# Performance work log

Measured on AMD Instinct MI355X. Metric: run time of the kernel, lower is better.

Reference implementation:

```python
import jax, jax.numpy as jnp
import numpy as np

H, C = 2, 128           # heads, out_channels per head
HC = H * C              # 256 concat output dim
D_IN = 256              # in_channels
D_T = 128               # time encoder out_channels
D_MSG = 128
E_DIM = D_MSG + D_T     # edge_dim = 256
N = 50000
E = 200000
MEAN_DT, STD_DT = 0.0, 1.0
SQRT_C = np.float32(np.sqrt(C))


def _time_enc(rel_t, W_t, b_t):
    # TGN TimeEncoder: cos(Linear(rel_t.view(-1,1)))  -> [E, D_T]
    return jnp.cos(rel_t[:, None] * W_t[0] + b_t)


def _seg_softmax(alpha, dst, n_dst):
    # numerically stable scatter-softmax over destination-node segments
    amax = jax.ops.segment_max(alpha, dst, num_segments=n_dst)
    amax = jnp.where(jnp.isfinite(amax), amax, 0.0)
    ex = jnp.exp(alpha - amax[dst])
    denom = jax.ops.segment_sum(ex, dst, num_segments=n_dst)
    return ex / (denom[dst] + 1e-16)


def _transformer_conv(x_src, x_dst, ei, edge_attr, Wq, bq, Wk, bk, Wv, bv, We, Ws, bs):
    n_dst = x_dst.shape[0]
    src, dst = ei[0], ei[1]
    q = (x_dst @ Wq + bq).reshape(n_dst, H, C)
    k = ((x_src @ Wk + bk)[src]).reshape(-1, H, C)      # gather per edge
    v = ((x_src @ Wv + bv)[src]).reshape(-1, H, C)
    e = (edge_attr @ We).reshape(-1, H, C)              # lin_edge (no bias)
    alpha = jnp.sum(q[dst] * (k + e), axis=-1) / SQRT_C  # [E, H]
    alpha = _seg_softmax(alpha, dst, n_dst)
    msg = (v + e) * alpha[..., None]                    # [E, H, C]
    out = jax.ops.segment_sum(msg.reshape(-1, HC), dst, num_segments=n_dst)
    return out + x_dst @ Ws + bs                        # root/skip connection


def setup_inputs() -> dict:
    key = jax.random.key(0)
    ks = jax.random.split(key, 32)
    s = 0.05
    inp = {
        'x_user': jax.random.normal(ks[0], (N, D_IN), jnp.float32),
        'x_item': jax.random.normal(ks[1], (N, D_IN), jnp.float32),
        'last_update_user': jax.random.uniform(ks[2], (N,), jnp.float32) * 100.0,
        'last_update_item': jax.random.uniform(ks[3], (N,), jnp.float32) * 100.0,
        'edge_index_a': jax.random.randint(ks[4], (2, E), 0, N, jnp.int32),
        'edge_index_b': jax.random.randint(ks[5], (2, E), 0, N, jnp.int32),
        't_a': jax.random.uniform(ks[6], (E,), jnp.float32) * 100.0 + 100.0,
        't_b': jax.random.uniform(ks[7], (E,), jnp.float32) * 100.0 + 100.0,
        'msg_a': jax.random.normal(ks[8], (E, D_MSG), jnp.float32),
        'msg_b': jax.random.normal(ks[9], (E, D_MSG), jnp.float32),
        'W_t': jax.random.normal(ks[10], (1, D_T), jnp.float32) * s,
        'b_t': jax.random.normal(ks[11], (D_T,), jnp.float32) * s,
    }
    i = 12
    for suf in ('a', 'b'):
        for nm, shape in (('Wq', (D_IN, HC)), ('bq', (HC,)), ('Wk', (D_IN, HC)), ('bk', (HC,)),
                          ('Wv', (D_IN, HC)), ('bv', (HC,)), ('We', (E_DIM, HC)),
                          ('Ws', (D_IN, HC)), ('bs', (HC,))):
            inp[f'{nm}_{suf}'] = jax.random.normal(ks[i], shape, jnp.float32) * s
            i += 1
    return inp


def reference(x_user, x_item, last_update_user, last_update_item,
              edge_index_a, edge_index_b, t_a, t_b, msg_a, msg_b, W_t, b_t,
              Wq_a, bq_a, Wk_a, bk_a, Wv_a, bv_a, We_a, Ws_a, bs_a,
              Wq_b, bq_b, Wk_b, bk_b, Wv_b, bv_b, We_b, Ws_b, bs_b):
    # edge type a: ('user','to','item');  edge type b: ('item','rev_to','user')
    rel_a = (t_a - last_update_user[edge_index_a[0]] - MEAN_DT) / STD_DT
    ea = jnp.concatenate([_time_enc(rel_a, W_t, b_t), msg_a], axis=-1)
    rel_b = (t_b - last_update_item[edge_index_b[0]] - MEAN_DT) / STD_DT
    eb = jnp.concatenate([_time_enc(rel_b, W_t, b_t), msg_b], axis=-1)
    out_item = _transformer_conv(x_user, x_item, edge_index_a, ea,
                                 Wq_a, bq_a, Wk_a, bk_a, Wv_a, bv_a, We_a, Ws_a, bs_a)
    out_user = _transformer_conv(x_item, x_user, edge_index_b, eb,
                                 Wq_b, bq_b, Wk_b, bk_b, Wv_b, bv_b, We_b, Ws_b, bs_b)
    return out_user, out_item
```

## Files before the change

kernel.cpp:

```cpp
#include <hip/hip_runtime.h>
#include <hip/hip_bf16.h>

#define N_NODES 50000
#define E_EDGES 200000
static constexpr float INV_SQRT_C = 0.08838834764831845f;
static constexpr int NB_NODE = ((N_NODES + 63) / 64) * 4;
static constexpr int NB_EDGE = E_EDGES / 64;
static constexpr int NB_PAIR = 2 * NB_EDGE;
static constexpr int NB_FUSED = NB_NODE + NB_EDGE;

typedef __attribute__((ext_vector_type(4))) float f32x4;
typedef __attribute__((ext_vector_type(8))) short s16x8;
typedef __attribute__((ext_vector_type(4))) short s16x4;

__device__ __forceinline__ float b2f(unsigned short u) {
  union { unsigned u; float f; } x; x.u = ((unsigned)u) << 16; return x.f;
}
__device__ __forceinline__ short f2b(float f) {
  union { float f; unsigned u; } x; x.f = f;
  unsigned r = x.u + 0x7FFFu + ((x.u >> 16) & 1u);
  return (short)(r >> 16);
}

struct WPtrs { const float* w[10]; };

__global__ __launch_bounds__(256) void prep_transpose(WPtrs p, short* __restrict__ out) {
  __shared__ short T[256 * 66];
  const int wi = blockIdx.x >> 2, cq = blockIdx.x & 3;
  const float* w = p.w[wi];
  short* o = out + wi * 65536;
  const int tid = threadIdx.x;
#pragma unroll
  for (int i = 0; i < 64; ++i) {
    int flat = tid + i * 256;
    int k = flat >> 6, cc = flat & 63;
    T[k * 66 + cc] = f2b(w[k * 256 + cq * 64 + cc]);
  }
  __syncthreads();
#pragma unroll
  for (int i = 0; i < 8; ++i) {
    int flat2 = tid + i * 256;
    int g = flat2 & 3, colb = (flat2 >> 2) & 15, ks = (flat2 >> 6) & 7, ctl = flat2 >> 9;
    int ct = cq * 4 + ctl;
    s16x8 v;
#pragma unroll
    for (int j = 0; j < 8; ++j)
      v[j] = T[(ks * 32 + g * 8 + j) * 66 + ctl * 16 + colb];
    *(s16x8*)(o + (((ct * 8 + ks) * 16 + colb) * 32 + g * 8)) = v;
  }
}

__global__ __launch_bounds__(256) void conv_x(const float* __restrict__ xu,
                                              const float* __restrict__ xi,
                                              unsigned short* __restrict__ x16u,
                                              unsigned short* __restrict__ x16i) {
  const float* in = blockIdx.y ? xi : xu;
  unsigned short* out = blockIdx.y ? x16i : x16u;
  size_t base = ((size_t)blockIdx.x * 256 + threadIdx.x) * 8;
  float4 a = *(const float4*)(in + base);
  float4 b = *(const float4*)(in + base + 4);
  s16x8 v;
  v[0] = f2b(a.x); v[1] = f2b(a.y); v[2] = f2b(a.z); v[3] = f2b(a.w);
  v[4] = f2b(b.x); v[5] = f2b(b.y); v[6] = f2b(b.z); v[7] = f2b(b.w);
  *(s16x8*)(out + base) = v;
}

__global__ __launch_bounds__(256) void csr_count2(const int* __restrict__ eia,
                                                  const int* __restrict__ eib,
                                                  int* __restrict__ counts) {
  int t = blockIdx.x * 256 + threadIdx.x;
  const int* ei = blockIdx.y ? eib : eia;
  int* c = counts + blockIdx.y * N_NODES;
  if (t < E_EDGES) atomicAdd(&c[ei[E_EDGES + t]], 1);
}

__global__ __launch_bounds__(1024) void csr_scan2(int* __restrict__ counts,
                                                  int* __restrict__ start) {
  int* cnt = counts + blockIdx.x * N_NODES;
  int* st  = start + blockIdx.x * (N_NODES + 1);
  __shared__ int wsum[16];
  __shared__ int chunk_tot;
  __shared__ int carry_s;
  const int tid = threadIdx.x, lane = tid & 63, wid = tid >> 6;
  if (tid == 0) carry_s = 0;
  __syncthreads();
  for (int base = 0; base < N_NODES; base += 1024) {
    int gi = base + tid;
    int x = (gi < N_NODES) ? cnt[gi] : 0;
    int v = x;
#pragma unroll
    for (int d = 1; d < 64; d <<= 1) {
      int t = __shfl_up(v, d);
      if (lane >= d) v += t;
    }
    if (lane == 63) wsum[wid] = v;
    __syncthreads();
    if (tid == 0) {
      int run = 0;
#pragma unroll
      for (int i = 0; i < 16; ++i) { int t = wsum[i]; wsum[i] = run; run += t; }
      chunk_tot = run;
    }
    __syncthreads();
    if (gi < N_NODES) {
      int excl = carry_s + wsum[wid] + v - x;
      st[gi] = excl;
      cnt[gi] = excl;
    }
    __syncthreads();
    if (tid == 0) carry_s += chunk_tot;
  }
  if (tid == 0) st[N_NODES] = carry_s;
}

__global__ __launch_bounds__(256) void csr_fill2(const int* __restrict__ eia,
                                                 const int* __restrict__ eib,
                                                 int* __restrict__ counts,
                                                 int* __restrict__ pos,
                                                 unsigned short* __restrict__ esrc) {
  int t = blockIdx.x * 256 + threadIdx.x;
  const int* ei = blockIdx.y ? eib : eia;
  int* cur = counts + blockIdx.y * N_NODES;
  int* ps  = pos + blockIdx.y * E_EDGES;
  unsigned short* es = esrc + (size_t)blockIdx.y * E_EDGES;
  if (t < E_EDGES) {
    int d = ei[E_EDGES + t];
    int p = atomicAdd(&cur[d], 1);
    ps[t] = p;
    es[p] = (unsigned short)ei[t];
  }
}

struct FusedArgs {
  const unsigned short* X16[4];
  const float* Xf[4];
  const short* Wt[4];
  const float* bias[4];
  unsigned short* o16[4];
  float* of[4];
  int use16;
  const int* ei; const float* tvec; const float* lu; const float* msg;
  const float* Wtim; const float* btim; const short* WeT; const int* pos;
  unsigned short* e16g;
};

__global__ __launch_bounds__(512) void fused_ne(FusedArgs A) {
  __shared__ __align__(16) char smem[34816];
  const int bx = blockIdx.x;
  const int tid = threadIdx.x;
  const int l = tid & 63;
  const int w = tid >> 6;
  const int colb = l & 15;
  const int g = l >> 4;

  int nb = -1, eb = -1;
  if (bx < NB_PAIR) { if (bx & 1) eb = bx >> 1; else nb = bx >> 1; }
  else nb = NB_EDGE + (bx - NB_PAIR);

  if (nb >= 0) {
    short* As = (short*)smem;
    const int job = nb / 782;
    const int m0 = (nb - job * 782) * 64;
    const bool fullblk = (m0 + 64 <= N_NODES);
    const short* Wt = A.Wt[job];
    const float* bias = A.bias[job];
    unsigned short* o16 = A.o16[job];
    float* of = A.of[job];

    if (A.use16) {
      const unsigned short* X = A.X16[job];
      if (fullblk) {
#pragma unroll
        for (int i = 0; i < 4; ++i) {
          int flat = tid + i * 512;
          int r = flat >> 5, cg = flat & 31;
          *(s16x8*)&As[r * 264 + cg * 8] = *(const s16x8*)(X + (size_t)(m0 + r) * 256 + cg * 8);
        }
      } else {
#pragma unroll
        for (int i = 0; i < 4; ++i) {
          int flat = tid + i * 512;
          int r = flat >> 5, cg = flat & 31;
          s16x8 v = (s16x8)(short)0;
          if (m0 + r < N_NODES) v = *(const s16x8*)(X + (size_t)(m0 + r) * 256 + cg * 8);
          *(s16x8*)&As[r * 264 + cg * 8] = v;
        }
      }
    } else {
      const float* X = A.Xf[job];
#pragma unroll
      for (int i = 0; i < 8; ++i) {
        int flat = tid + i * 512;
        int r = flat >> 6, c4 = flat & 63;
        float4 xv = make_float4(0.f, 0.f, 0.f, 0.f);
        if (fullblk || m0 + r < N_NODES) xv = *(const float4*)(X + (size_t)(m0 + r) * 256 + c4 * 4);
        s16x4 sv; sv[0] = f2b(xv.x); sv[1] = f2b(xv.y); sv[2] = f2b(xv.z); sv[3] = f2b(xv.w);
        *(s16x4*)&As[r * 264 + c4 * 4] = sv;
      }
    }
    __syncthreads();

    const short* wbase0 = Wt + (((2 * w + 0) * 8) * 16 + colb) * 32 + g * 8;
    const short* wbase1 = Wt + (((2 * w + 1) * 8) * 16 + colb) * 32 + g * 8;

    f32x4 acc[4][2];
#pragma unroll
    for (int m = 0; m < 4; ++m) { acc[m][0] = (f32x4)(0.0f); acc[m][1] = (f32x4)(0.0f); }
#pragma unroll
    for (int ks = 0; ks < 8; ++ks) {
      s16x8 b0 = *(const s16x8*)(wbase0 + ks * 512);
      s16x8 b1 = *(const s16x8*)(wbase1 + ks * 512);
#pragma unroll
      for (int m = 0; m < 4; ++m) {
        s16x8 a = *(const s16x8*)&As[(16 * m + colb) * 264 + ks * 32 + g * 8];
        acc[m][0] = __builtin_amdgcn_mfma_f32_16x16x32_bf16(a, b0, acc[m][0], 0, 0, 0);
        acc[m][1] = __builtin_amdgcn_mfma_f32_16x16x32_bf16(a, b1, acc[m][1], 0, 0, 0);
      }
    }
    __syncthreads();

    if (of) {
      float* buf = (float*)smem;
#pragma unroll 1
      for (int half = 0; half < 2; ++half) {
#pragma unroll
        for (int j = 0; j < 2; ++j) {
          int col = (2 * w + j) * 16 + colb;
          float bv = bias[col];
#pragma unroll
          for (int mm = 0; mm < 2; ++mm) {
            int m = half * 2 + mm;
#pragma unroll
            for (int r = 0; r < 4; ++r)
              buf[(16 * mm + g * 4 + r) * 260 + col] = acc[m][j][r] + bv;
          }
        }
        __syncthreads();
#pragma unroll
        for (int i = 0; i < 4; ++i) {
          int flat = tid + i * 512;
          int row = flat >> 6, ch = flat & 63;
          int grow = m0 + half * 32 + row;
          if (fullblk || grow < N_NODES)
            *(float4*)(of + (size_t)grow * 256 + ch * 4) = *(const float4*)&buf[row * 260 + ch * 4];
        }
        __syncthreads();
      }
    } else {
      short* buf = (short*)smem;
#pragma unroll
      for (int j = 0; j < 2; ++j) {
        int col = (2 * w + j) * 16 + colb;
        float bv = bias[col];
#pragma unroll
        for (int m = 0; m < 4; ++m)
#pragma unroll
          for (int r = 0; r < 4; ++r)
            buf[(16 * m + g * 4 + r) * 264 + col] = f2b(acc[m][j][r] + bv);
      }
      __syncthreads();
#pragma unroll
      for (int i = 0; i < 4; ++i) {
        int flat = tid + i * 512;
        int row = flat >> 5, ch = flat & 31;
        if (fullblk || m0 + row < N_NODES)
          *(s16x8*)(o16 + (size_t)(m0 + row) * 256 + ch * 8) = *(const s16x8*)&buf[row * 264 + ch * 8];
      }
    }
  } else {
    short* attr = (short*)smem;
    float* rel  = (float*)(smem + 33792);
    int*   poss = (int*)(smem + 34048);
    const int e0 = eb * 64;

    const float wt = A.Wtim[tid & 127], bt = A.btim[tid & 127];

    if (tid < 64) {
      rel[tid] = A.tvec[e0 + tid] - A.lu[A.ei[e0 + tid]];
      poss[tid] = A.pos[e0 + tid];
    }
#pragma unroll
    for (int i = 0; i < 4; ++i) {
      int flat = tid + i * 512;
      int row = flat >> 5, c4 = flat & 31;
      float4 mv = *(const float4*)(A.msg + (size_t)(e0 + row) * 128 + c4 * 4);
      s16x4 sv; sv[0] = f2b(mv.x); sv[1] = f2b(mv.y); sv[2] = f2b(mv.z); sv[3] = f2b(mv.w);
      *(s16x4*)&attr[row * 264 + 128 + c4 * 4] = sv;
    }
    __syncthreads();

    {
      int col = tid & 127;
      int r0 = (tid >> 7) * 16;
#pragma unroll
      for (int i = 0; i < 16; ++i)
        attr[(r0 + i) * 264 + col] = f2b(__cosf(rel[r0 + i] * wt + bt));
    }
    __syncthreads();

    const short* wbase0 = A.WeT + (((2 * w + 0) * 8) * 16 + colb) * 32 + g * 8;
    const short* wbase1 = A.WeT + (((2 * w + 1) * 8) * 16 + colb) * 32 + g * 8;
    f32x4 acc[4][2];
#pragma unroll
    for (int m = 0; m < 4; ++m) { acc[m][0] = (f32x4)(0.0f); acc[m][1] = (f32x4)(0.0f); }
#pragma unroll
    for (int ks = 0; ks < 8; ++ks) {
      s16x8 b0 = *(const s16x8*)(wbase0 + ks * 512);
      s16x8 b1 = *(const s16x8*)(wbase1 + ks * 512);
#pragma unroll
      for (int m = 0; m < 4; ++m) {
        s16x8 a = *(const s16x8*)&attr[(16 * m + colb) * 264 + ks * 32 + g * 8];
        acc[m][0] = __builtin_amdgcn_mfma_f32_16x16x32_bf16(a, b0, acc[m][0], 0, 0, 0);
        acc[m][1] = __builtin_amdgcn_mfma_f32_16x16x32_bf16(a, b1, acc[m][1], 0, 0, 0);
      }
    }
    __syncthreads();
#pragma unroll
    for (int j = 0; j < 2; ++j)
#pragma unroll
      for (int m = 0; m < 4; ++m)
#pragma unroll
        for (int r = 0; r < 4; ++r)
          attr[(16 * m + g * 4 + r) * 264 + (2 * w + j) * 16 + colb] = f2b(acc[m][j][r]);
    __syncthreads();

#pragma unroll
    for (int i = 0; i < 4; ++i) {
      int flat = tid + i * 512;
      int row = flat >> 5, cg = flat & 31;
      size_t slot = (size_t)poss[row];
      *(s16x8*)(A.e16g + slot * 256 + cg * 8) = *(const s16x8*)&attr[row * 264 + cg * 8];
    }
  }
}

__global__ __launch_bounds__(256) void aggregate_fused5(
    const int* __restrict__ start, const unsigned short* __restrict__ esrc,
    const unsigned short* __restrict__ Q16, const unsigned short* __restrict__ K16,
    const unsigned short* __restrict__ V16, const unsigned short* __restrict__ e16,
    float* __restrict__ out)
{
  const int wave = blockIdx.x * 4 + (threadIdx.x >> 6);
  const int nwaves = gridDim.x * 4;
  const int lane = threadIdx.x & 63;
  const int c0 = lane * 4;

  for (int d = wave; d < N_NODES; d += nwaves) {
    const int s0 = start[d], s1 = start[d + 1];
    if (s1 <= s0) continue;

    s16x4 qv = *(const s16x4*)(Q16 + (size_t)d * 256 + c0);
    const float q0 = b2f((unsigned short)qv[0]), q1 = b2f((unsigned short)qv[1]);
    const float q2 = b2f((unsigned short)qv[2]), q3 = b2f((unsigned short)qv[3]);

    float den = 0.f;
    float a0 = 0.f, a1 = 0.f, a2 = 0.f, a3 = 0.f;
    int p = s0;

#define EDGE_LOAD(J, PP)                                                    \
    int s##J = (int)esrc[PP];                                               \
    s16x4 ev##J = *(const s16x4*)(e16 + (size_t)(PP) * 256 + c0);           \
    s16x4 kv##J = *(const s16x4*)(K16 + (size_t)s##J * 256 + c0);           \
    s16x4 vv##J = *(const s16x4*)(V16 + (size_t)s##J * 256 + c0);           \
    float e0##J = b2f((unsigned short)ev##J[0]), e1##J = b2f((unsigned short)ev##J[1]); \
    float e2##J = b2f((unsigned short)ev##J[2]), e3##J = b2f((unsigned short)ev##J[3]); \
    float dt##J = q0 * (b2f((unsigned short)kv##J[0]) + e0##J)              \
                + q1 * (b2f((unsigned short)kv##J[1]) + e1##J)              \
                + q2 * (b2f((unsigned short)kv##J[2]) + e2##J)              \
                + q3 * (b2f((unsigned short)kv##J[3]) + e3##J);

#define EDGE_ACC(J)                                                         \
    den += ex##J;                                                           \
    a0 += ex##J * (b2f((unsigned short)vv##J[0]) + e0##J);                  \
    a1 += ex##J * (b2f((unsigned short)vv##J[1]) + e1##J);                  \
    a2 += ex##J * (b2f((unsigned short)vv##J[2]) + e2##J);                  \
    a3 += ex##J * (b2f((unsigned short)vv##J[3]) + e3##J);

    for (; p + 4 <= s1; p += 4) {
      EDGE_LOAD(A, p)  EDGE_LOAD(B, p + 1)  EDGE_LOAD(C, p + 2)  EDGE_LOAD(D, p + 3)
      dtA += __shfl_xor(dtA, 1);  dtB += __shfl_xor(dtB, 1);
      dtC += __shfl_xor(dtC, 1);  dtD += __shfl_xor(dtD, 1);
      dtA += __shfl_xor(dtA, 2);  dtB += __shfl_xor(dtB, 2);
      dtC += __shfl_xor(dtC, 2);  dtD += __shfl_xor(dtD, 2);
      dtA += __shfl_xor(dtA, 4);  dtB += __shfl_xor(dtB, 4);
      dtC += __shfl_xor(dtC, 4);  dtD += __shfl_xor(dtD, 4);
      dtA += __shfl_xor(dtA, 8);  dtB += __shfl_xor(dtB, 8);
      dtC += __shfl_xor(dtC, 8);  dtD += __shfl_xor(dtD, 8);
      dtA += __shfl_xor(dtA, 16); dtB += __shfl_xor(dtB, 16);
      dtC += __shfl_xor(dtC, 16); dtD += __shfl_xor(dtD, 16);
      float exA = __expf(dtA * INV_SQRT_C), exB = __expf(dtB * INV_SQRT_C);
      float exC = __expf(dtC * INV_SQRT_C), exD = __expf(dtD * INV_SQRT_C);
      EDGE_ACC(A) EDGE_ACC(B) EDGE_ACC(C) EDGE_ACC(D)
    }
    for (; p < s1; ++p) {
      EDGE_LOAD(T, p)
      dtT += __shfl_xor(dtT, 1);
      dtT += __shfl_xor(dtT, 2);
      dtT += __shfl_xor(dtT, 4);
      dtT += __shfl_xor(dtT, 8);
      dtT += __shfl_xor(dtT, 16);
      float exT = __expf(dtT * INV_SQRT_C);
      EDGE_ACC(T)
    }
#undef EDGE_LOAD
#undef EDGE_ACC

    float inv = 1.f / (den + 1e-16f);
    float4* op = (float4*)(out + (size_t)d * 256 + c0);
    float4 o = *op;
    o.x += a0 * inv; o.y += a1 * inv; o.z += a2 * inv; o.w += a3 * inv;
    *op = o;
  }
}

extern "C" void kernel_launch(void* const* d_in, const int* in_sizes, int n_in,
                              void* d_out, int out_size, void* d_ws, size_t ws_size,
                              hipStream_t stream) {
  const float* x_user  = (const float*)d_in[0];
  const float* x_item  = (const float*)d_in[1];
  const float* lu_user = (const float*)d_in[2];
  const float* lu_item = (const float*)d_in[3];
  const int*   ei_a    = (const int*)d_in[4];
  const int*   ei_b    = (const int*)d_in[5];
  const float* t_a     = (const float*)d_in[6];
  const float* t_b     = (const float*)d_in[7];
  const float* msg_a   = (const float*)d_in[8];
  const float* msg_b   = (const float*)d_in[9];
  const float* W_t     = (const float*)d_in[10];
  const float* b_t     = (const float*)d_in[11];
  const float* Wq_a = (const float*)d_in[12]; const float* bq_a = (const float*)d_in[13];
  const float* Wk_a = (const float*)d_in[14]; const float* bk_a = (const float*)d_in[15];
  const float* Wv_a = (const float*)d_in[16]; const float* bv_a = (const float*)d_in[17];
  const float* We_a = (const float*)d_in[18];
  const float* Ws_a = (const float*)d_in[19]; const float* bs_a = (const float*)d_in[20];
  const float* Wq_b = (const float*)d_in[21]; const float* bq_b = (const float*)d_in[22];
  const float* Wk_b = (const float*)d_in[23]; const float* bk_b = (const float*)d_in[24];
  const float* Wv_b = (const float*)d_in[25]; const float* bv_b = (const float*)d_in[26];
  const float* We_b = (const float*)d_in[27];
  const float* Ws_b = (const float*)d_in[28]; const float* bs_b = (const float*)d_in[29];

  float* out_user = (float*)d_out;
  float* out_item = (float*)d_out + (size_t)N_NODES * 256;

  WPtrs wp;
  wp.w[0] = Wq_a; wp.w[1] = Wk_a; wp.w[2] = Wv_a; wp.w[3] = Ws_a; wp.w[4] = We_a;
  wp.w[5] = Wq_b; wp.w[6] = Wk_b; wp.w[7] = Wv_b; wp.w[8] = Ws_b; wp.w[9] = We_b;

  dim3 blk(256);
  dim3 blk512(512);
  dim3 gW(40);
  dim3 gF(NB_FUSED);
  dim3 gEt2((E_EDGES + 255) / 256, 2);
  dim3 gAgg(1024);
  dim3 gCv(6250, 2);

  char* ws = (char*)d_ws;
  size_t off = 0;
  short* WtT = (short*)(ws + off); off += (size_t)10 * 65536 * 2;
  unsigned short* Q16 = (unsigned short*)(ws + off); off += (size_t)N_NODES * 256 * 2;
  unsigned short* K16 = (unsigned short*)(ws + off); off += (size_t)N_NODES * 256 * 2;
  unsigned short* V16 = (unsigned short*)(ws + off); off += (size_t)N_NODES * 256 * 2;
  unsigned short* e16 = (unsigned short*)(ws + off); off += (size_t)E_EDGES * 256 * 2;
  int* pos    = (int*)(ws + off); off += (size_t)2 * E_EDGES * 4;
  int* counts = (int*)(ws + off); off += (size_t)2 * N_NODES * 4;
  int* startb = (int*)(ws + off); off += (size_t)2 * (N_NODES + 1) * 4;
  unsigned short* esrc = (unsigned short*)(ws + off); off += (size_t)2 * E_EDGES * 2;
  const size_t off_base = off;
  unsigned short* X16u = (unsigned short*)(ws + off); off += (size_t)N_NODES * 256 * 2;
  unsigned short* X16i = (unsigned short*)(ws + off); off += (size_t)N_NODES * 256 * 2;
  const bool use_x16 = (ws_size >= off);
  if (!use_x16 && ws_size < off_base) return;

  prep_transpose<<<gW, blk, 0, stream>>>(wp, WtT);

  hipMemsetAsync(counts, 0, (size_t)2 * N_NODES * 4, stream);
  csr_count2<<<gEt2, blk, 0, stream>>>(ei_a, ei_b, counts);
  csr_scan2<<<2, 1024, 0, stream>>>(counts, startb);
  csr_fill2<<<gEt2, blk, 0, stream>>>(ei_a, ei_b, counts, pos, esrc);

  if (use_x16)
    conv_x<<<gCv, blk, 0, stream>>>(x_user, x_item, X16u, X16i);

  {
    FusedArgs Aa;
    Aa.X16[0] = X16u; Aa.X16[1] = X16u; Aa.X16[2] = X16i; Aa.X16[3] = X16i;
    Aa.Xf[0] = x_user; Aa.Xf[1] = x_user; Aa.Xf[2] = x_item; Aa.Xf[3] = x_item;
    Aa.Wt[0] = WtT + 1 * 65536; Aa.Wt[1] = WtT + 2 * 65536;
    Aa.Wt[2] = WtT + 0 * 65536; Aa.Wt[3] = WtT + 3 * 65536;
    Aa.bias[0] = bk_a; Aa.bias[1] = bv_a; Aa.bias[2] = bq_a; Aa.bias[3] = bs_a;
    Aa.o16[0] = K16; Aa.o16[1] = V16; Aa.o16[2] = Q16; Aa.o16[3] = nullptr;
    Aa.of[0] = nullptr; Aa.of[1] = nullptr; Aa.of[2] = nullptr; Aa.of[3] = out_item;
    Aa.use16 = use_x16 ? 1 : 0;
    Aa.ei = ei_a; Aa.tvec = t_a; Aa.lu = lu_user; Aa.msg = msg_a;
    Aa.Wtim = W_t; Aa.btim = b_t; Aa.WeT = WtT + 4 * 65536; Aa.pos = pos;
    Aa.e16g = e16;
    fused_ne<<<gF, blk512, 0, stream>>>(Aa);
  }
  aggregate_fused5<<<gAgg, blk, 0, stream>>>(startb, esrc, Q16, K16, V16, e16, out_item);

  {
    FusedArgs Ab;
    Ab.X16[0] = X16i; Ab.X16[1] = X16i; Ab.X16[2] = X16u; Ab.X16[3] = X16u;
    Ab.Xf[0] = x_item; Ab.Xf[1] = x_item; Ab.Xf[2] = x_user; Ab.Xf[3] = x_user;
    Ab.Wt[0] = WtT + 6 * 65536; Ab.Wt[1] = WtT + 7 * 65536;
    Ab.Wt[2] = WtT + 5 * 65536; Ab.Wt[3] = WtT + 8 * 65536;
    Ab.bias[0] = bk_b; Ab.bias[1] = bv_b; Ab.bias[2] = bq_b; Ab.bias[3] = bs_b;
    Ab.o16[0] = K16; Ab.o16[1] = V16; Ab.o16[2] = Q16; Ab.o16[3] = nullptr;
    Ab.of[0] = nullptr; Ab.of[1] = nullptr; Ab.of[2] = nullptr; Ab.of[3] = out_user;
    Ab.use16 = use_x16 ? 1 : 0;
    Ab.ei = ei_b; Ab.tvec = t_b; Ab.lu = lu_item; Ab.msg = msg_b;
    Ab.Wtim = W_t; Ab.btim = b_t; Ab.WeT = WtT + 9 * 65536; Ab.pos = pos + E_EDGES;
    Ab.e16g = e16;
    fused_ne<<<gF, blk512, 0, stream>>>(Ab);
  }
  aggregate_fused5<<<gAgg, blk, 0, stream>>>(startb + (N_NODES + 1), esrc + E_EDGES,
      Q16, K16, V16, e16, out_user);
}
```

Baseline: 587.0 us.

## Merge both edge types into single projection and aggregation kernels

Adds a second set of Q/K/V/edge-feature workspace buffers so both edge types can be processed together. Their projection GEMMs then run in one mega_ne launch and their aggregations in one mega_agg launch, interleaving destinations of both types. Weight transpose, bf16 conversion of x and CSR counting are folded into a single setup kernel. The aim is to remove launch gaps and serialization between the two convolutions and fill the GPU better, at the cost of more workspace memory, with a fallback to the old path when workspace is too small.

```diff
diff --git a/kernel.cpp b/kernel.cpp
--- a/kernel.cpp
+++ b/kernel.cpp
@@ -8,6 +8,9 @@
 static constexpr int NB_EDGE = E_EDGES / 64;
 static constexpr int NB_PAIR = 2 * NB_EDGE;
 static constexpr int NB_FUSED = NB_NODE + NB_EDGE;
+static constexpr int NB_PREP = 40;
+static constexpr int NB_CONV = 12500;
+static constexpr int NB_CNT  = ((E_EDGES + 255) / 256) * 2;
 
 typedef __attribute__((ext_vector_type(4))) float f32x4;
 typedef __attribute__((ext_vector_type(8))) short s16x8;
@@ -24,53 +27,335 @@
 
 struct WPtrs { const float* w[10]; };
 
-__global__ __launch_bounds__(256) void prep_transpose(WPtrs p, short* __restrict__ out) {
+struct NodeSet {
+  const unsigned short* X16[4];
+  const float* Xf[4];
+  const short* Wt[4];
+  const float* bias[4];
+  unsigned short* o16[4];
+  float* of[4];
+};
+struct EdgeSet {
+  const int* ei; const float* tvec; const float* lu; const float* msg;
+  const short* WeT; const int* pos; unsigned short* e16g;
+};
+
+__device__ __forceinline__ void node_block(char* smem, int tid, int nb,
+                                           const NodeSet& N, int use16) {
+  short* As = (short*)smem;
+  const int l = tid & 63;
+  const int w = tid >> 6;
+  const int colb = l & 15;
+  const int g = l >> 4;
+  const int job = nb / 782;
+  const int m0 = (nb - job * 782) * 64;
+  const bool fullblk = (m0 + 64 <= N_NODES);
+  const short* Wt = N.Wt[job];
+  const float* bias = N.bias[job];
+  unsigned short* o16 = N.o16[job];
+  float* of = N.of[job];
+
+  if (use16) {
+    const unsigned short* X = N.X16[job];
+    if (fullblk) {
+#pragma unroll
+      for (int i = 0; i < 4; ++i) {
+        int flat = tid + i * 512;
+        int r = flat >> 5, cg = flat & 31;
+        *(s16x8*)&As[r * 264 + cg * 8] = *(const s16x8*)(X + (size_t)(m0 + r) * 256 + cg * 8);
+      }
+    } else {
+#pragma unroll
+      for (int i = 0; i < 4; ++i) {
+        int flat = tid + i * 512;
+        int r = flat >> 5, cg = flat & 31;
+        s16x8 v = (s16x8)(short)0;
+        if (m0 + r < N_NODES) v = *(const s16x8*)(X + (size_t)(m0 + r) * 256 + cg * 8);
+        *(s16x8*)&As[r * 264 + cg * 8] = v;
+      }
+    }
+  } else {
+    const float* X = N.Xf[job];
+#pragma unroll
+    for (int i = 0; i < 8; ++i) {
+      int flat = tid + i * 512;
+      int r = flat >> 6, c4 = flat & 63;
+      float4 xv = make_float4(0.f, 0.f, 0.f, 0.f);
+      if (fullblk || m0 + r < N_NODES) xv = *(const float4*)(X + (size_t)(m0 + r) * 256 + c4 * 4);
+      s16x4 sv; sv[0] = f2b(xv.x); sv[1] = f2b(xv.y); sv[2] = f2b(xv.z); sv[3] = f2b(xv.w);
+      *(s16x4*)&As[r * 264 + c4 * 4] = sv;
+    }
+  }
+  __syncthreads();
+
+  const short* wbase0 = Wt + (((2 * w + 0) * 8) * 16 + colb) * 32 + g * 8;
+  const short* wbase1 = Wt + (((2 * w + 1) * 8) * 16 + colb) * 32 + g * 8;
+
+  f32x4 acc[4][2];
+#pragma unroll
+  for (int m = 0; m < 4; ++m) { acc[m][0] = (f32x4)(0.0f); acc[m][1] = (f32x4)(0.0f); }
+#pragma unroll
+  for (int ks = 0; ks < 8; ++ks) {
+    s16x8 b0 = *(const s16x8*)(wbase0 + ks * 512);
+    s16x8 b1 = *(const s16x8*)(wbase1 + ks * 512);
+#pragma unroll
+    for (int m = 0; m < 4; ++m) {
+      s16x8 a = *(const s16x8*)&As[(16 * m + colb) * 264 + ks * 32 + g * 8];
+      acc[m][0] = __builtin_amdgcn_mfma_f32_16x16x32_bf16(a, b0, acc[m][0], 0, 0, 0);
+      acc[m][1] = __builtin_amdgcn_mfma_f32_16x16x32_bf16(a, b1, acc[m][1], 0, 0, 0);
+    }
+  }
+  __syncthreads();
+
+  if (of) {
+    float* buf = (float*)smem;
+#pragma unroll 1
+    for (int half = 0; half < 2; ++half) {
+#pragma unroll
+      for (int j = 0; j < 2; ++j) {
+        int col = (2 * w + j) * 16 + colb;
+        float bv = bias[col];
+#pragma unroll
+        for (int mm = 0; mm < 2; ++mm) {
+          int m = half * 2 + mm;
+#pragma unroll
+          for (int r = 0; r < 4; ++r)
+            buf[(16 * mm + g * 4 + r) * 260 + col] = acc[m][j][r] + bv;
+        }
+      }
+      __syncthreads();
+#pragma unroll
+      for (int i = 0; i < 4; ++i) {
+        int flat = tid + i * 512;
+        int row = flat >> 6, ch = flat & 63;
+        int grow = m0 + half * 32 + row;
+        if (fullblk || grow < N_NODES)
+          *(float4*)(of + (size_t)grow * 256 + ch * 4) = *(const float4*)&buf[row * 260 + ch * 4];
+      }
+      __syncthreads();
+    }
+  } else {
+    short* buf = (short*)smem;
+#pragma unroll
+    for (int j = 0; j < 2; ++j) {
+      int col = (2 * w + j) * 16 + colb;
+      float bv = bias[col];
+#pragma unroll
+      for (int m = 0; m < 4; ++m)
+#pragma unroll
+        for (int r = 0; r < 4; ++r)
+          buf[(16 * m + g * 4 + r) * 264 + col] = f2b(acc[m][j][r] + bv);
+    }
+    __syncthreads();
+#pragma unroll
+    for (int i = 0; i < 4; ++i) {
+      int flat = tid + i * 512;
+      int row = flat >> 5, ch = flat & 31;
+      if (fullblk || m0 + row < N_NODES)
+        *(s16x8*)(o16 + (size_t)(m0 + row) * 256 + ch * 8) = *(const s16x8*)&buf[row * 264 + ch * 8];
+    }
+  }
+}
+
+__device__ __forceinline__ void edge_block(char* smem, int tid, int eb,
+                                           const EdgeSet& E,
+                                           const float* Wtim, const float* btim) {
+  short* attr = (short*)smem;
+  float* rel  = (float*)(smem + 33792);
+  int*   poss = (int*)(smem + 34048);
+  const int l = tid & 63;
+  const int w = tid >> 6;
+  const int colb = l & 15;
+  const int g = l >> 4;
+  const int e0 = eb * 64;
+
+  const float wt = Wtim[tid & 127], bt = btim[tid & 127];
+
+  if (tid < 64) {
+    rel[tid] = E.tvec[e0 + tid] - E.lu[E.ei[e0 + tid]];
+    poss[tid] = E.pos[e0 + tid];
+  }
+#pragma unroll
+  for (int i = 0; i < 4; ++i) {
+    int flat = tid + i * 512;
+    int row = flat >> 5, c4 = flat & 31;
+    float4 mv = *(const float4*)(E.msg + (size_t)(e0 + row) * 128 + c4 * 4);
+    s16x4 sv; sv[0] = f2b(mv.x); sv[1] = f2b(mv.y); sv[2] = f2b(mv.z); sv[3] = f2b(mv.w);
+    *(s16x4*)&attr[row * 264 + 128 + c4 * 4] = sv;
+  }
+  __syncthreads();
+
+  {
+    int col = tid & 127;
+    int r0 = (tid >> 7) * 16;
+#pragma unroll
+    for (int i = 0; i < 16; ++i)
+      attr[(r0 + i) * 264 + col] = f2b(__cosf(rel[r0 + i] * wt + bt));
+  }
+  __syncthreads();
+
+  const short* wbase0 = E.WeT + (((2 * w + 0) * 8) * 16 + colb) * 32 + g * 8;
+  const short* wbase1 = E.WeT + (((2 * w + 1) * 8) * 16 + colb) * 32 + g * 8;
+  f32x4 acc[4][2];
+#pragma unroll
+  for (int m = 0; m < 4; ++m) { acc[m][0] = (f32x4)(0.0f); acc[m][1] = (f32x4)(0.0f); }
+#pragma unroll
+  for (int ks = 0; ks < 8; ++ks) {
+    s16x8 b0 = *(const s16x8*)(wbase0 + ks * 512);
+    s16x8 b1 = *(const s16x8*)(wbase1 + ks * 512);
+#pragma unroll
+    for (int m = 0; m < 4; ++m) {
+      s16x8 a = *(const s16x8*)&attr[(16 * m + colb) * 264 + ks * 32 + g * 8];
+      acc[m][0] = __builtin_amdgcn_mfma_f32_16x16x32_bf16(a, b0, acc[m][0], 0, 0, 0);
+      acc[m][1] = __builtin_amdgcn_mfma_f32_16x16x32_bf16(a, b1, acc[m][1], 0, 0, 0);
+    }
+  }
+  __syncthreads();
+#pragma unroll
+  for (int j = 0; j < 2; ++j)
+#pragma unroll
+    for (int m = 0; m < 4; ++m)
+#pragma unroll
+      for (int r = 0; r < 4; ++r)
+        attr[(16 * m + g * 4 + r) * 264 + (2 * w + j) * 16 + colb] = f2b(acc[m][j][r]);
+  __syncthreads();
+
+#pragma unroll
+  for (int i = 0; i < 4; ++i) {
+    int flat = tid + i * 512;
+    int row = flat >> 5, cg = flat & 31;
+    size_t slot = (size_t)poss[row];
+    *(s16x8*)(E.e16g + slot * 256 + cg * 8) = *(const s16x8*)&attr[row * 264 + cg * 8];
+  }
+}
+
+__device__ __forceinline__ void process_dst(
+    int d, int c0, const int* __restrict__ start, const unsigned short* __restrict__ esrc,
+    const unsigned short* __restrict__ Q16, const unsigned short* __restrict__ K16,
+    const unsigned short* __restrict__ V16, const unsigned short* __restrict__ e16,
+    float* __restrict__ out)
+{
+  const int s0 = start[d], s1 = start[d + 1];
+  if (s1 <= s0) return;
+
+  s16x4 qv = *(const s16x4*)(Q16 + (size_t)d * 256 + c0);
+  const float q0 = b2f((unsigned short)qv[0]), q1 = b2f((unsigned short)qv[1]);
+  const float q2 = b2f((unsigned short)qv[2]), q3 = b2f((unsigned short)qv[3]);
+
+  float den = 0.f;
+  float a0 = 0.f, a1 = 0.f, a2 = 0.f, a3 = 0.f;
+  int p = s0;
+
+#define EDGE_LOAD(J, PP)                                                    \
+    int s##J = (int)esrc[PP];                                               \
+    s16x4 ev##J = *(const s16x4*)(e16 + (size_t)(PP) * 256 + c0);           \
+    s16x4 kv##J = *(const s16x4*)(K16 + (size_t)s##J * 256 + c0);           \
+    s16x4 vv##J = *(const s16x4*)(V16 + (size_t)s##J * 256 + c0);           \
+    float e0##J = b2f((unsigned short)ev##J[0]), e1##J = b2f((unsigned short)ev##J[1]); \
+    float e2##J = b2f((unsigned short)ev##J[2]), e3##J = b2f((unsigned short)ev##J[3]); \
+    float dt##J = q0 * (b2f((unsigned short)kv##J[0]) + e0##J)              \
+                + q1 * (b2f((unsigned short)kv##J[1]) + e1##J)              \
+                + q2 * (b2f((unsigned short)kv##J[2]) + e2##J)              \
+                + q3 * (b2f((unsigned short)kv##J[3]) + e3##J);
+
+#define EDGE_ACC(J)                                                         \
+    den += ex##J;                                                           \
+    a0 += ex##J * (b2f((unsigned short)vv##J[0]) + e0##J);                  \
+    a1 += ex##J * (b2f((unsigned short)vv##J[1]) + e1##J);                  \
+    a2 += ex##J * (b2f((unsigned short)vv##J[2]) + e2##J);                  \
+    a3 += ex##J * (b2f((unsigned short)vv##J[3]) + e3##J);
+
+  for (; p + 4 <= s1; p += 4) {
+    EDGE_LOAD(A, p)  EDGE_LOAD(B, p + 1)  EDGE_LOAD(C, p + 2)  EDGE_LOAD(D, p + 3)
+    dtA += __shfl_xor(dtA, 1);  dtB += __shfl_xor(dtB, 1);
+    dtC += __shfl_xor(dtC, 1);  dtD += __shfl_xor(dtD, 1);
+    dtA += __shfl_xor(dtA, 2);  dtB += __shfl_xor(dtB, 2);
+    dtC += __shfl_xor(dtC, 2);  dtD += __shfl_xor(dtD, 2);
+    dtA += __shfl_xor(dtA, 4);  dtB += __shfl_xor(dtB, 4);
+    dtC += __shfl_xor(dtC, 4);  dtD += __shfl_xor(dtD, 4);
+    dtA += __shfl_xor(dtA, 8);  dtB += __shfl_xor(dtB, 8);
+    dtC += __shfl_xor(dtC, 8);  dtD += __shfl_xor(dtD, 8);
+    dtA += __shfl_xor(dtA, 16); dtB += __shfl_xor(dtB, 16);
+    dtC += __shfl_xor(dtC, 16); dtD += __shfl_xor(dtD, 16);
+    float exA = __expf(dtA * INV_SQRT_C), exB = __expf(dtB * INV_SQRT_C);
+    float exC = __expf(dtC * INV_SQRT_C), exD = __expf(dtD * INV_SQRT_C);
+    EDGE_ACC(A) EDGE_ACC(B) EDGE_ACC(C) EDGE_ACC(D)
+  }
+  for (; p < s1; ++p) {
+    EDGE_LOAD(T, p)
+    dtT += __shfl_xor(dtT, 1);
+    dtT += __shfl_xor(dtT, 2);
+    dtT += __shfl_xor(dtT, 4);
+    dtT += __shfl_xor(dtT, 8);
+    dtT += __shfl_xor(dtT, 16);
+    float exT = __expf(dtT * INV_SQRT_C);
+    EDGE_ACC(T)
+  }
+#undef EDGE_LOAD
+#undef EDGE_ACC
+
+  float inv = 1.f / (den + 1e-16f);
+  float4* op = (float4*)(out + (size_t)d * 256 + c0);
+  float4 o = *op;
+  o.x += a0 * inv; o.y += a1 * inv; o.z += a2 * inv; o.w += a3 * inv;
+  *op = o;
+}
+
+__global__ __launch_bounds__(256) void setup_fused(
+    WPtrs p, short* __restrict__ WtT,
+    const float* __restrict__ xu, const float* __restrict__ xi,
+    unsigned short* __restrict__ x16u, unsigned short* __restrict__ x16i, int nconv,
+    const int* __restrict__ eia, const int* __restrict__ eib, int* __restrict__ counts)
+{
   __shared__ short T[256 * 66];
-  const int wi = blockIdx.x >> 2, cq = blockIdx.x & 3;
-  const float* w = p.w[wi];
-  short* o = out + wi * 65536;
+  const int bx = blockIdx.x;
   const int tid = threadIdx.x;
-#pragma unroll
-  for (int i = 0; i < 64; ++i) {
-    int flat = tid + i * 256;
-    int k = flat >> 6, cc = flat & 63;
-    T[k * 66 + cc] = f2b(w[k * 256 + cq * 64 + cc]);
-  }
-  __syncthreads();
-#pragma unroll
-  for (int i = 0; i < 8; ++i) {
-    int flat2 = tid + i * 256;
-    int g = flat2 & 3, colb = (flat2 >> 2) & 15, ks = (flat2 >> 6) & 7, ctl = flat2 >> 9;
-    int ct = cq * 4 + ctl;
+
+  if (bx < NB_PREP) {
+    const int wi = bx >> 2, cq = bx & 3;
+    const float* w = p.w[wi];
+    short* o = WtT + wi * 65536;
+#pragma unroll
+    for (int i = 0; i < 64; ++i) {
+      int flat = tid + i * 256;
+      int k = flat >> 6, cc = flat & 63;
+      T[k * 66 + cc] = f2b(w[k * 256 + cq * 64 + cc]);
+    }
+    __syncthreads();
+#pragma unroll
+    for (int i = 0; i < 8; ++i) {
+      int flat2 = tid + i * 256;
+      int g = flat2 & 3, colb = (flat2 >> 2) & 15, ks = (flat2 >> 6) & 7, ctl = flat2 >> 9;
+      int ct = cq * 4 + ctl;
+      s16x8 v;
+#pragma unroll
+      for (int j = 0; j < 8; ++j)
+        v[j] = T[(ks * 32 + g * 8 + j) * 66 + ctl * 16 + colb];
+      *(s16x8*)(o + (((ct * 8 + ks) * 16 + colb) * 32 + g * 8)) = v;
+    }
+    return;
+  }
+  int cb = bx - NB_PREP;
+  if (cb < nconv) {
+    int y = cb >= (nconv / 2);
+    int xb = y ? cb - nconv / 2 : cb;
+    const float* in = y ? xi : xu;
+    unsigned short* out = y ? x16i : x16u;
+    size_t base = ((size_t)xb * 256 + tid) * 8;
+    float4 a = *(const float4*)(in + base);
+    float4 b = *(const float4*)(in + base + 4);
     s16x8 v;
-#pragma unroll
-    for (int j = 0; j < 8; ++j)
-      v[j] = T[(ks * 32 + g * 8 + j) * 66 + ctl * 16 + colb];
-    *(s16x8*)(o + (((ct * 8 + ks) * 16 + colb) * 32 + g * 8)) = v;
-  }
-}
-
-__global__ __launch_bounds__(256) void conv_x(const float* __restrict__ xu,
-                                              const float* __restrict__ xi,
-                                              unsigned short* __restrict__ x16u,
-                                              unsigned short* __restrict__ x16i) {
-  const float* in = blockIdx.y ? xi : xu;
-  unsigned short* out = blockIdx.y ? x16i : x16u;
-  size_t base = ((size_t)blockIdx.x * 256 + threadIdx.x) * 8;
-  float4 a = *(const float4*)(in + base);
-  float4 b = *(const float4*)(in + base + 4);
-  s16x8 v;
-  v[0] = f2b(a.x); v[1] = f2b(a.y); v[2] = f2b(a.z); v[3] = f2b(a.w);
-  v[4] = f2b(b.x); v[5] = f2b(b.y); v[6] = f2b(b.z); v[7] = f2b(b.w);
-  *(s16x8*)(out + base) = v;
-}
-
-__global__ __launch_bounds__(256) void csr_count2(const int* __restrict__ eia,
-                                                  const int* __restrict__ eib,
-                                                  int* __restrict__ counts) {
-  int t = blockIdx.x * 256 + threadIdx.x;
-  const int* ei = blockIdx.y ? eib : eia;
-  int* c = counts + blockIdx.y * N_NODES;
+    v[0] = f2b(a.x); v[1] = f2b(a.y); v[2] = f2b(a.z); v[3] = f2b(a.w);
+    v[4] = f2b(b.x); v[5] = f2b(b.y); v[6] = f2b(b.z); v[7] = f2b(b.w);
+    *(s16x8*)(out + base) = v;
+    return;
+  }
+  cb -= nconv;
+  int y = cb >= (NB_CNT / 2);
+  int tb = y ? cb - NB_CNT / 2 : cb;
+  const int* ei = y ? eib : eia;
+  int* c = counts + y * N_NODES;
+  int t = tb * 256 + tid;
   if (t < E_EDGES) atomicAdd(&c[ei[E_EDGES + t]], 1);
 }
 
@@ -131,207 +416,29 @@
   }
 }
 
-struct FusedArgs {
-  const unsigned short* X16[4];
-  const float* Xf[4];
-  const short* Wt[4];
-  const float* bias[4];
-  unsigned short* o16[4];
-  float* of[4];
-  int use16;
-  const int* ei; const float* tvec; const float* lu; const float* msg;
-  const float* Wtim; const float* btim; const short* WeT; const int* pos;
-  unsigned short* e16g;
-};
+struct FusedArgs { NodeSet n; EdgeSet e; const float* Wtim; const float* btim; int use16; };
 
 __global__ __launch_bounds__(512) void fused_ne(FusedArgs A) {
   __shared__ __align__(16) char smem[34816];
   const int bx = blockIdx.x;
-  const int tid = threadIdx.x;
-  const int l = tid & 63;
-  const int w = tid >> 6;
-  const int colb = l & 15;
-  const int g = l >> 4;
-
   int nb = -1, eb = -1;
   if (bx < NB_PAIR) { if (bx & 1) eb = bx >> 1; else nb = bx >> 1; }
   else nb = NB_EDGE + (bx - NB_PAIR);
-
-  if (nb >= 0) {
-    short* As = (short*)smem;
-    const int job = nb / 782;
-    const int m0 = (nb - job * 782) * 64;
-    const bool fullblk = (m0 + 64 <= N_NODES);
-    const short* Wt = A.Wt[job];
-    const float* bias = A.bias[job];
-    unsigned short* o16 = A.o16[job];
-    float* of = A.of[job];
-
-    if (A.use16) {
-      const unsigned short* X = A.X16[job];
-      if (fullblk) {
-#pragma unroll
-        for (int i = 0; i < 4; ++i) {
-          int flat = tid + i * 512;
-          int r = flat >> 5, cg = flat & 31;
-          *(s16x8*)&As[r * 264 + cg * 8] = *(const s16x8*)(X + (size_t)(m0 + r) * 256 + cg * 8);
-        }
-      } else {
-#pragma unroll
-        for (int i = 0; i < 4; ++i) {
-          int flat = tid + i * 512;
-          int r = flat >> 5, cg = flat & 31;
-          s16x8 v = (s16x8)(short)0;
-          if (m0 + r < N_NODES) v = *(const s16x8*)(X + (size_t)(m0 + r) * 256 + cg * 8);
-          *(s16x8*)&As[r * 264 + cg * 8] = v;
-        }
-      }
-    } else {
-      const float* X = A.Xf[job];
-#pragma unroll
-      for (int i = 0; i < 8; ++i) {
-        int flat = tid + i * 512;
-        int r = flat >> 6, c4 = flat & 63;
-        float4 xv = make_float4(0.f, 0.f, 0.f, 0.f);
-        if (fullblk || m0 + r < N_NODES) xv = *(const float4*)(X + (size_t)(m0 + r) * 256 + c4 * 4);
-        s16x4 sv; sv[0] = f2b(xv.x); sv[1] = f2b(xv.y); sv[2] = f2b(xv.z); sv[3] = f2b(xv.w);
-        *(s16x4*)&As[r * 264 + c4 * 4] = sv;
-      }
-    }
-    __syncthreads();
-
-    const short* wbase0 = Wt + (((2 * w + 0) * 8) * 16 + colb) * 32 + g * 8;
-    const short* wbase1 = Wt + (((2 * w + 1) * 8) * 16 + colb) * 32 + g * 8;
-
-    f32x4 acc[4][2];
-#pragma unroll
-    for (int m = 0; m < 4; ++m) { acc[m][0] = (f32x4)(0.0f); acc[m][1] = (f32x4)(0.0f); }
-#pragma unroll
-    for (int ks = 0; ks < 8; ++ks) {
-      s16x8 b0 = *(const s16x8*)(wbase0 + ks * 512);
-      s16x8 b1 = *(const s16x8*)(wbase1 + ks * 512);
-#pragma unroll
-      for (int m = 0; m < 4; ++m) {
-        s16x8 a = *(const s16x8*)&As[(16 * m + colb) * 264 + ks * 32 + g * 8];
-        acc[m][0] = __builtin_amdgcn_mfma_f32_16x16x32_bf16(a, b0, acc[m][0], 0, 0, 0);
-        acc[m][1] = __builtin_amdgcn_mfma_f32_16x16x32_bf16(a, b1, acc[m][1], 0, 0, 0);
-      }
-    }
-    __syncthreads();
-
-    if (of) {
-      float* buf = (float*)smem;
-#pragma unroll 1
-      for (int half = 0; half < 2; ++half) {
-#pragma unroll
-        for (int j = 0; j < 2; ++j) {
-          int col = (2 * w + j) * 16 + colb;
-          float bv = bias[col];
-#pragma unroll
-          for (int mm = 0; mm < 2; ++mm) {
-            int m = half * 2 + mm;
-#pragma unroll
-            for (int r = 0; r < 4; ++r)
-              buf[(16 * mm + g * 4 + r) * 260 + col] = acc[m][j][r] + bv;
-          }
-        }
-        __syncthreads();
-#pragma unroll
-        for (int i = 0; i < 4; ++i) {
-          int flat = tid + i * 512;
-          int row = flat >> 6, ch = flat & 63;
-          int grow = m0 + half * 32 + row;
-          if (fullblk || grow < N_NODES)
-            *(float4*)(of + (size_t)grow * 256 + ch * 4) = *(const float4*)&buf[row * 260 + ch * 4];
-        }
-        __syncthreads();
-      }
-    } else {
-      short* buf = (short*)smem;
-#pragma unroll
-      for (int j = 0; j < 2; ++j) {
-        int col = (2 * w + j) * 16 + colb;
-        float bv = bias[col];
-#pragma unroll
-        for (int m = 0; m < 4; ++m)
-#pragma unroll
-          for (int r = 0; r < 4; ++r)
-            buf[(16 * m + g * 4 + r) * 264 + col] = f2b(acc[m][j][r] + bv);
-      }
-      __syncthreads();
-#pragma unroll
-      for (int i = 0; i < 4; ++i) {
-        int flat = tid + i * 512;
-        int row = flat >> 5, ch = flat & 31;
-        if (fullblk || m0 + row < N_NODES)
-          *(s16x8*)(o16 + (size_t)(m0 + row) * 256 + ch * 8) = *(const s16x8*)&buf[row * 264 + ch * 8];
-      }
-    }
-  } else {
-    short* attr = (short*)smem;
-    float* rel  = (float*)(smem + 33792);
-    int*   poss = (int*)(smem + 34048);
-    const int e0 = eb * 64;
-
-    const float wt = A.Wtim[tid & 127], bt = A.btim[tid & 127];
-
-    if (tid < 64) {
-      rel[tid] = A.tvec[e0 + tid] - A.lu[A.ei[e0 + tid]];
-      poss[tid] = A.pos[e0 + tid];
-    }
-#pragma unroll
-    for (int i = 0; i < 4; ++i) {
-      int flat = tid + i * 512;
-      int row = flat >> 5, c4 = flat & 31;
-      float4 mv = *(const float4*)(A.msg + (size_t)(e0 + row) * 128 + c4 * 4);
-      s16x4 sv; sv[0] = f2b(mv.x); sv[1] = f2b(mv.y); sv[2] = f2b(mv.z); sv[3] = f2b(mv.w);
-      *(s16x4*)&attr[row * 264 + 128 + c4 * 4] = sv;
-    }
-    __syncthreads();
-
-    {
-      int col = tid & 127;
-      int r0 = (tid >> 7) * 16;
-#pragma unroll
-      for (int i = 0; i < 16; ++i)
-        attr[(r0 + i) * 264 + col] = f2b(__cosf(rel[r0 + i] * wt + bt));
-    }
-    __syncthreads();
-
-    const short* wbase0 = A.WeT + (((2 * w + 0) * 8) * 16 + colb) * 32 + g * 8;
-    const short* wbase1 = A.WeT + (((2 * w + 1) * 8) * 16 + colb) * 32 + g * 8;
-    f32x4 acc[4][2];
-#pragma unroll
-    for (int m = 0; m < 4; ++m) { acc[m][0] = (f32x4)(0.0f); acc[m][1] = (f32x4)(0.0f); }
-#pragma unroll
-    for (int ks = 0; ks < 8; ++ks) {
-      s16x8 b0 = *(const s16x8*)(wbase0 + ks * 512);
-      s16x8 b1 = *(const s16x8*)(wbase1 + ks * 512);
-#pragma unroll
-      for (int m = 0; m < 4; ++m) {
-        s16x8 a = *(const s16x8*)&attr[(16 * m + colb) * 264 + ks * 32 + g * 8];
-        acc[m][0] = __builtin_amdgcn_mfma_f32_16x16x32_bf16(a, b0, acc[m][0], 0, 0, 0);
-        acc[m][1] = __builtin_amdgcn_mfma_f32_16x16x32_bf16(a, b1, acc[m][1], 0, 0, 0);
-      }
-    }
-    __syncthreads();
-#pragma unroll
-    for (int j = 0; j < 2; ++j)
-#pragma unroll
-      for (int m = 0; m < 4; ++m)
-#pragma unroll
-        for (int r = 0; r < 4; ++r)
-          attr[(16 * m + g * 4 + r) * 264 + (2 * w + j) * 16 + colb] = f2b(acc[m][j][r]);
-    __syncthreads();
-
-#pragma unroll
-    for (int i = 0; i < 4; ++i) {
-      int flat = tid + i * 512;
-      int row = flat >> 5, cg = flat & 31;
-      size_t slot = (size_t)poss[row];
-      *(s16x8*)(A.e16g + slot * 256 + cg * 8) = *(const s16x8*)&attr[row * 264 + cg * 8];
-    }
-  }
+  if (nb >= 0) node_block(smem, threadIdx.x, nb, A.n, A.use16);
+  else         edge_block(smem, threadIdx.x, eb, A.e, A.Wtim, A.btim);
+}
+
+struct MegaNE { NodeSet n[2]; EdgeSet e[2]; const float* Wtim; const float* btim; int use16; };
+
+__global__ __launch_bounds__(512) void mega_ne(MegaNE M) {
+  __shared__ __align__(16) char smem[34816];
+  const int type = blockIdx.x / NB_FUSED;
+  const int bx = blockIdx.x - type * NB_FUSED;
+  int nb = -1, eb = -1;
+  if (bx < NB_PAIR) { if (bx & 1) eb = bx >> 1; else nb = bx >> 1; }
+  else nb = NB_EDGE + (bx - NB_PAIR);
+  if (nb >= 0) node_block(smem, threadIdx.x, nb, M.n[type], M.use16);
+  else         edge_block(smem, threadIdx.x, eb, M.e[type], M.Wtim, M.btim);
 }
 
 __global__ __launch_bounds__(256) void aggregate_fused5(
@@ -342,74 +449,27 @@
 {
   const int wave = blockIdx.x * 4 + (threadIdx.x >> 6);
   const int nwaves = gridDim.x * 4;
-  const int lane = threadIdx.x & 63;
-  const int c0 = lane * 4;
-
-  for (int d = wave; d < N_NODES; d += nwaves) {
-    const int s0 = start[d], s1 = start[d + 1];
-    if (s1 <= s0) continue;
-
-    s16x4 qv = *(const s16x4*)(Q16 + (size_t)d * 256 + c0);
-    const float q0 = b2f((unsigned short)qv[0]), q1 = b2f((unsigned short)qv[1]);
-    const float q2 = b2f((unsigned short)qv[2]), q3 = b2f((unsigned short)qv[3]);
-
-    float den = 0.f;
-    float a0 = 0.f, a1 = 0.f, a2 = 0.f, a3 = 0.f;
-    int p = s0;
-
-#define EDGE_LOAD(J, PP)                                                    \
-    int s##J = (int)esrc[PP];                                               \
-    s16x4 ev##J = *(const s16x4*)(e16 + (size_t)(PP) * 256 + c0);           \
-    s16x4 kv##J = *(const s16x4*)(K16 + (size_t)s##J * 256 + c0);           \
-    s16x4 vv##J = *(const s16x4*)(V16 + (size_t)s##J * 256 + c0);           \
-    float e0##J = b2f((unsigned short)ev##J[0]), e1##J = b2f((unsigned short)ev##J[1]); \
-    float e2##J = b2f((unsigned short)ev##J[2]), e3##J = b2f((unsigned short)ev##J[3]); \
-    float dt##J = q0 * (b2f((unsigned short)kv##J[0]) + e0##J)              \
-                + q1 * (b2f((unsigned short)kv##J[1]) + e1##J)              \
-                + q2 * (b2f((unsigned short)kv##J[2]) + e2##J)              \
-                + q3 * (b2f((unsigned short)kv##J[3]) + e3##J);
-
-#define EDGE_ACC(J)                                                         \
-    den += ex##J;                                                           \
-    a0 += ex##J * (b2f((unsigned short)vv##J[0]) + e0##J);                  \
-    a1 += ex##J * (b2f((unsigned short)vv##J[1]) + e1##J);                  \
-    a2 += ex##J * (b2f((unsigned short)vv##J[2]) + e2##J);                  \
-    a3 += ex##J * (b2f((unsigned short)vv##J[3]) + e3##J);
-
-    for (; p + 4 <= s1; p += 4) {
-      EDGE_LOAD(A, p)  EDGE_LOAD(B, p + 1)  EDGE_LOAD(C, p + 2)  EDGE_LOAD(D, p + 3)
-      dtA += __shfl_xor(dtA, 1);  dtB += __shfl_xor(dtB, 1);
-      dtC += __shfl_xor(dtC, 1);  dtD += __shfl_xor(dtD, 1);
-      dtA += __shfl_xor(dtA, 2);  dtB += __shfl_xor(dtB, 2);
-      dtC += __shfl_xor(dtC, 2);  dtD += __shfl_xor(dtD, 2);
-      dtA += __shfl_xor(dtA, 4);  dtB += __shfl_xor(dtB, 4);
-      dtC += __shfl_xor(dtC, 4);  dtD += __shfl_xor(dtD, 4);
-      dtA += __shfl_xor(dtA, 8);  dtB += __shfl_xor(dtB, 8);
-      dtC += __shfl_xor(dtC, 8);  dtD += __shfl_xor(dtD, 8);
-      dtA += __shfl_xor(dtA, 16); dtB += __shfl_xor(dtB, 16);
-      dtC += __shfl_xor(dtC, 16); dtD += __shfl_xor(dtD, 16);
-      float exA = __expf(dtA * INV_SQRT_C), exB = __expf(dtB * INV_SQRT_C);
-      float exC = __expf(dtC * INV_SQRT_C), exD = __expf(dtD * INV_SQRT_C);
-      EDGE_ACC(A) EDGE_ACC(B) EDGE_ACC(C) EDGE_ACC(D)
-    }
-    for (; p < s1; ++p) {
-      EDGE_LOAD(T, p)
-      dtT += __shfl_xor(dtT, 1);
-      dtT += __shfl_xor(dtT, 2);
-      dtT += __shfl_xor(dtT, 4);
-      dtT += __shfl_xor(dtT, 8);
-      dtT += __shfl_xor(dtT, 16);
-      float exT = __expf(dtT * INV_SQRT_C);
-      EDGE_ACC(T)
-    }
-#undef EDGE_LOAD
-#undef EDGE_ACC
-
-    float inv = 1.f / (den + 1e-16f);
-    float4* op = (float4*)(out + (size_t)d * 256 + c0);
-    float4 o = *op;
-    o.x += a0 * inv; o.y += a1 * inv; o.z += a2 * inv; o.w += a3 * inv;
-    *op = o;
+  const int c0 = (threadIdx.x & 63) * 4;
+  for (int d = wave; d < N_NODES; d += nwaves)
+    process_dst(d, c0, start, esrc, Q16, K16, V16, e16, out);
+}
+
+struct MegaAgg {
+  const int* start[2]; const unsigned short* esrc[2];
+  const unsigned short* Q[2]; const unsigned short* K[2];
+  const unsigned short* V[2]; const unsigned short* e16[2];
+  float* out[2];
+};
+
+__global__ __launch_bounds__(256) void mega_agg(MegaAgg G) {
+  const int wave = blockIdx.x * 4 + (threadIdx.x >> 6);
+  const int nwaves = gridDim.x * 4;
+  const int c0 = (threadIdx.x & 63) * 4;
+  for (int dg = wave; dg < 2 * N_NODES; dg += nwaves) {
+    const int type = dg & 1;
+    const int d = dg >> 1;
+    process_dst(d, c0, G.start[type], G.esrc[type], G.Q[type], G.K[type],
+                G.V[type], G.e16[type], G.out[type]);
   }
 }
 
@@ -448,19 +508,16 @@
 
   dim3 blk(256);
   dim3 blk512(512);
-  dim3 gW(40);
-  dim3 gF(NB_FUSED);
   dim3 gEt2((E_EDGES + 255) / 256, 2);
   dim3 gAgg(1024);
-  dim3 gCv(6250, 2);
 
   char* ws = (char*)d_ws;
   size_t off = 0;
   short* WtT = (short*)(ws + off); off += (size_t)10 * 65536 * 2;
-  unsigned short* Q16 = (unsigned short*)(ws + off); off += (size_t)N_NODES * 256 * 2;
-  unsigned short* K16 = (unsigned short*)(ws + off); off += (size_t)N_NODES * 256 * 2;
-  unsigned short* V16 = (unsigned short*)(ws + off); off += (size_t)N_NODES * 256 * 2;
-  unsigned short* e16 = (unsigned short*)(ws + off); off += (size_t)E_EDGES * 256 * 2;
+  unsigned short* Q16a = (unsigned short*)(ws + off); off += (size_t)N_NODES * 256 * 2;
+  unsigned short* K16a = (unsigned short*)(ws + off); off += (size_t)N_NODES * 256 * 2;
+  unsigned short* V16a = (unsigned short*)(ws + off); off += (size_t)N_NODES * 256 * 2;
+  unsigned short* e16a = (unsigned short*)(ws + off); off += (size_t)E_EDGES * 256 * 2;
   int* pos    = (int*)(ws + off); off += (size_t)2 * E_EDGES * 4;
   int* counts = (int*)(ws + off); off += (size_t)2 * N_NODES * 4;
   int* startb = (int*)(ws + off); off += (size_t)2 * (N_NODES + 1) * 4;
@@ -468,51 +525,69 @@
   const size_t off_base = off;
   unsigned short* X16u = (unsigned short*)(ws + off); off += (size_t)N_NODES * 256 * 2;
   unsigned short* X16i = (unsigned short*)(ws + off); off += (size_t)N_NODES * 256 * 2;
-  const bool use_x16 = (ws_size >= off);
+  const size_t off_t1 = off;
+  unsigned short* Q16b = (unsigned short*)(ws + off); off += (size_t)N_NODES * 256 * 2;
+  unsigned short* K16b = (unsigned short*)(ws + off); off += (size_t)N_NODES * 256 * 2;
+  unsigned short* V16b = (unsigned short*)(ws + off); off += (size_t)N_NODES * 256 * 2;
+  unsigned short* e16b = (unsigned short*)(ws + off); off += (size_t)E_EDGES * 256 * 2;
+  const size_t off_t2 = off;
+  const bool use_x16 = (ws_size >= off_t1);
+  const bool use_t2  = (ws_size >= off_t2);
   if (!use_x16 && ws_size < off_base) return;
 
-  prep_transpose<<<gW, blk, 0, stream>>>(wp, WtT);
+  const int nconv = use_x16 ? NB_CONV : 0;
 
   hipMemsetAsync(counts, 0, (size_t)2 * N_NODES * 4, stream);
-  csr_count2<<<gEt2, blk, 0, stream>>>(ei_a, ei_b, counts);
+  setup_fused<<<dim3(NB_PREP + nconv + NB_CNT), blk, 0, stream>>>(
+      wp, WtT, x_user, x_item, X16u, X16i, nconv, ei_a, ei_b, counts);
   csr_scan2<<<2, 1024, 0, stream>>>(counts, startb);
   csr_fill2<<<gEt2, blk, 0, stream>>>(ei_a, ei_b, counts, pos, esrc);
 
-  if (use_x16)
-    conv_x<<<gCv, blk, 0, stream>>>(x_user, x_item, X16u, X16i);
-
-  {
-    FusedArgs Aa;
-    Aa.X16[0] = X16u; Aa.X16[1] = X16u; Aa.X16[2] = X16i; Aa.X16[3] = X16i;
-    Aa.Xf[0] = x_user; Aa.Xf[1] = x_user; Aa.Xf[2] = x_item; Aa.Xf[3] = x_item;
-    Aa.Wt[0] = WtT + 1 * 65536; Aa.Wt[1] = WtT + 2 * 65536;
-    Aa.Wt[2] = WtT + 0 * 65536; Aa.Wt[3] = WtT + 3 * 65536;
-    Aa.bias[0] = bk_a; Aa.bias[1] = bv_a; Aa.bias[2] = bq_a; Aa.bias[3] = bs_a;
-    Aa.o16[0] = K16; Aa.o16[1] = V16; Aa.o16[2] = Q16; Aa.o16[3] = nullptr;
-    Aa.of[0] = nullptr; Aa.of[1] = nullptr; Aa.of[2] = nullptr; Aa.of[3] = out_item;
-    Aa.use16 = use_x16 ? 1 : 0;
-    Aa.ei = ei_a; Aa.tvec = t_a; Aa.lu = lu_user; Aa.msg = msg_a;
-    Aa.Wtim = W_t; Aa.btim = b_t; Aa.WeT = WtT + 4 * 65536; Aa.pos = pos;
-    Aa.e16g = e16;
-    fused_ne<<<gF, blk512, 0, stream>>>(Aa);
-  }
-  aggregate_fused5<<<gAgg, blk, 0, stream>>>(startb, esrc, Q16, K16, V16, e16, out_item);
-
-  {
-    FusedArgs Ab;
-    Ab.X16[0] = X16i; Ab.X16[1] = X16i; Ab.X16[2] = X16u; Ab.X16[3] = X16u;
-    Ab.Xf[0] = x_item; Ab.Xf[1] = x_item; Ab.Xf[2] = x_user; Ab.Xf[3] = x_user;
-    Ab.Wt[0] = WtT + 6 * 65536; Ab.Wt[1] = WtT + 7 * 65536;
-    Ab.Wt[2] = WtT + 5 * 65536; Ab.Wt[3] = WtT + 8 * 65536;
-    Ab.bias[0] = bk_b; Ab.bias[1] = bv_b; Ab.bias[2] = bq_b; Ab.bias[3] = bs_b;
-    Ab.o16[0] = K16; Ab.o16[1] = V16; Ab.o16[2] = Q16; Ab.o16[3] = nullptr;
-    Ab.of[0] = nullptr; Ab.of[1] = nullptr; Ab.of[2] = nullptr; Ab.of[3] = out_user;
-    Ab.use16 = use_x16 ? 1 : 0;
-    Ab.ei = ei_b; Ab.tvec = t_b; Ab.lu = lu_item; Ab.msg = msg_b;
-    Ab.Wtim = W_t; Ab.btim = b_t; Ab.WeT = WtT + 9 * 65536; Ab.pos = pos + E_EDGES;
-    Ab.e16g = e16;
-    fused_ne<<<gF, blk512, 0, stream>>>(Ab);
-  }
-  aggregate_fused5<<<gAgg, blk, 0, stream>>>(startb + (N_NODES + 1), esrc + E_EDGES,
-      Q16, K16, V16, e16, out_user);
-}
+  NodeSet na, nb_;
+  na.X16[0] = X16u; na.X16[1] = X16u; na.X16[2] = X16i; na.X16[3] = X16i;
+  na.Xf[0] = x_user; na.Xf[1] = x_user; na.Xf[2] = x_item; na.Xf[3] = x_item;
+  na.Wt[0] = WtT + 1 * 65536; na.Wt[1] = WtT + 2 * 65536;
+  na.Wt[2] = WtT + 0 * 65536; na.Wt[3] = WtT + 3 * 65536;
+  na.bias[0] = bk_a; na.bias[1] = bv_a; na.bias[2] = bq_a; na.bias[3] = bs_a;
+  na.o16[0] = K16a; na.o16[1] = V16a; na.o16[2] = Q16a; na.o16[3] = nullptr;
+  na.of[0] = nullptr; na.of[1] = nullptr; na.of[2] = nullptr; na.of[3] = out_item;
+
+  nb_.X16[0] = X16i; nb_.X16[1] = X16i; nb_.X16[2] = X16u; nb_.X16[3] = X16u;
+  nb_.Xf[0] = x_item; nb_.Xf[1] = x_item; nb_.Xf[2] = x_user; nb_.Xf[3] = x_user;
+  nb_.Wt[0] = WtT + 6 * 65536; nb_.Wt[1] = WtT + 7 * 65536;
+  nb_.Wt[2] = WtT + 5 * 65536; nb_.Wt[3] = WtT + 8 * 65536;
+  nb_.bias[0] = bk_b; nb_.bias[1] = bv_b; nb_.bias[2] = bq_b; nb_.bias[3] = bs_b;
+  nb_.of[0] = nullptr; nb_.of[1] = nullptr; nb_.of[2] = nullptr; nb_.of[3] = out_user;
+
+  EdgeSet ea, eb_;
+  ea.ei = ei_a; ea.tvec = t_a; ea.lu = lu_user; ea.msg = msg_a;
+  ea.WeT = WtT + 4 * 65536; ea.pos = pos; ea.e16g = e16a;
+  eb_.ei = ei_b; eb_.tvec = t_b; eb_.lu = lu_item; eb_.msg = msg_b;
+  eb_.WeT = WtT + 9 * 65536; eb_.pos = pos + E_EDGES;
+
+  if (use_t2) {
+    nb_.o16[0] = K16b; nb_.o16[1] = V16b; nb_.o16[2] = Q16b;
+    eb_.e16g = e16b;
+    MegaNE M;
+    M.n[0] = na; M.n[1] = nb_; M.e[0] = ea; M.e[1] = eb_;
+    M.Wtim = W_t; M.btim = b_t; M.use16 = 1;
+    mega_ne<<<dim3(2 * NB_FUSED), blk512, 0, stream>>>(M);
+    MegaAgg G;
+    G.start[0] = startb; G.start[1] = startb + (N_NODES + 1);
+    G.esrc[0] = esrc;    G.esrc[1] = esrc + E_EDGES;
+    G.Q[0] = Q16a; G.Q[1] = Q16b; G.K[0] = K16a; G.K[1] = K16b;
+    G.V[0] = V16a; G.V[1] = V16b; G.e16[0] = e16a; G.e16[1] = e16b;
+    G.out[0] = out_item; G.out[1] = out_user;
+    mega_agg<<<dim3(2048), blk, 0, stream>>>(G);
+  } else {
+    nb_.o16[0] = K16a; nb_.o16[1] = V16a; nb_.o16[2] = Q16a;
+    eb_.e16g = e16a;
+    FusedArgs Aa; Aa.n = na; Aa.e = ea; Aa.Wtim = W_t; Aa.btim = b_t; Aa.use16 = use_x16 ? 1 : 0;
+    fused_ne<<<dim3(NB_FUSED), blk512, 0, stream>>>(Aa);
+    aggregate_fused5<<<gAgg, blk, 0, stream>>>(startb, esrc, Q16a, K16a, V16a, e16a, out_item);
+    FusedArgs Ab; Ab.n = nb_; Ab.e = eb_; Ab.Wtim = W_t; Ab.btim = b_t; Ab.use16 = use_x16 ? 1 : 0;
+    fused_ne<<<dim3(NB_FUSED), blk512, 0, stream>>>(Ab);
+    aggregate_fused5<<<gAgg, blk, 0, stream>>>(startb + (N_NODES + 1), esrc + E_EDGES,
+        Q16a, K16a, V16a, e16a, out_user);
+  }
+}
```

New measurement: 578.7 us. Within noise of the previous version (-1.4%).
